# Kernel optimization log

Hardware: AMD Instinct MI355X
Metric: run time of the kernel (lower is better)

Reference implementation:

```python
import jax, jax.numpy as jnp
import numpy as np
import math

B, S, D, H = 2, 1024, 1024, 16
DH = D // H
BUCKETS, MAXPOS = 256, 512
SPAN = BUCKETS  # pos_ebd_size (att_span)


def make_log_bucket_position(rel, bucket_size, max_position):
    sign = jnp.sign(rel).astype(jnp.float32)
    mid = bucket_size // 2
    abs_pos = jnp.where((rel < mid) & (rel > -mid), mid - 1, jnp.abs(rel)).astype(jnp.float32)
    log_pos = jnp.ceil(jnp.log(abs_pos / mid) / np.log((max_position - 1) / mid) * (mid - 1)) + mid
    return jnp.where(abs_pos <= mid, rel.astype(jnp.float32), log_pos * sign).astype(jnp.int32)


def build_relative_position(q_size, k_size):
    rel = jnp.arange(q_size, dtype=jnp.int32)[:, None] - jnp.arange(k_size, dtype=jnp.int32)[None, :]
    return make_log_bucket_position(rel, BUCKETS, MAXPOS)


def setup_inputs() -> dict:
    key = jax.random.key(0)
    ks = jax.random.split(key, 8)
    w = lambda k: jax.random.normal(k, (D, D), dtype=jnp.float32) * 0.02
    return {
        "hidden_states": jax.random.normal(ks[0], (B, S, D), dtype=jnp.float32),
        "attention_mask": jnp.ones((B, 1, S, S), dtype=jnp.int32),
        "rel_embeddings": jax.random.normal(ks[1], (2 * SPAN, D), dtype=jnp.float32),
        "Wq": w(ks[2]), "bq": jnp.zeros((D,), jnp.float32),
        "Wk": w(ks[3]), "bk": jnp.zeros((D,), jnp.float32),
        "Wv": w(ks[4]), "bv": jnp.zeros((D,), jnp.float32),
    }


def reference(hidden_states, attention_mask, rel_embeddings, Wq, bq, Wk, bk, Wv, bv):
    split = lambda x: x.reshape(B, -1, H, DH).transpose(0, 2, 1, 3)  # [B,H,S,dh]
    q = split(hidden_states @ Wq + bq)
    k = split(hidden_states @ Wk + bk)
    v = split(hidden_states @ Wv + bv)

    SCALE_FACTOR = 3  # 1 + c2p + p2c
    scale = math.sqrt(DH * SCALE_FACTOR)
    scores = jnp.einsum('bhqd,bhkd->bhqk', q, k) / scale

    # disentangled relative-position bias (share_att_key=True -> reuse q/k proj)
    re = rel_embeddings[: 2 * SPAN]  # [2*SPAN, D]
    pos_q = (re @ Wq + bq).reshape(2 * SPAN, H, DH).transpose(1, 0, 2)  # [H,P,dh]
    pos_k = (re @ Wk + bk).reshape(2 * SPAN, H, DH).transpose(1, 0, 2)

    rel_pos = build_relative_position(S, S)  # [S,S] bucketized

    # c2p: gather along the position axis per (q,k) pair
    c2p_pos = jnp.clip(rel_pos + SPAN, 0, 2 * SPAN - 1)
    c2p_att = jnp.einsum('bhqd,hpd->bhqp', q, pos_k)  # [B,H,S,2*SPAN]
    c2p = jnp.take_along_axis(c2p_att, c2p_pos[None, None], axis=-1)  # [B,H,S,S]

    # p2c: gather for key positions, then transpose back to [q,k]
    p2c_pos = jnp.clip(-rel_pos + SPAN, 0, 2 * SPAN - 1)
    p2c_att = jnp.einsum('bhkd,hpd->bhkp', k, pos_q)
    p2c = jnp.swapaxes(jnp.take_along_axis(p2c_att, p2c_pos[None, None], axis=-1), -1, -2)

    scores = scores + (c2p + p2c) / scale

    # XSoftmax: masked fill -> softmax -> zero masked
    valid = attention_mask.astype(bool)
    scores = jnp.where(valid, scores, jnp.finfo(scores.dtype).min)
    probs = jax.nn.softmax(scores, axis=-1)
    probs = jnp.where(valid, probs, 0.0)

    ctx = jnp.einsum('bhqk,bhkd->bhqd', probs, v)
    return ctx.transpose(0, 2, 1, 3).reshape(B, S, D)
```

## Files before the change

### kernel.cpp

```cpp
#include <hip/hip_runtime.h>
#include <hip/hip_bf16.h>
#include <math.h>

#define B_   2
#define S_   1024
#define D_   1024
#define H_   16
#define DH_  64
#define P_   512

#define SCALE2 (0.07216878364870323f * 1.4426950408889634f)

typedef __bf16 bf16;
typedef __bf16 bf16x8 __attribute__((ext_vector_type(8)));
typedef __bf16 bf16x4 __attribute__((ext_vector_type(4)));
typedef float  f32x4  __attribute__((ext_vector_type(4)));

__device__ __forceinline__ f32x4 mfma16(bf16x8 a, bf16x8 b, f32x4 c) {
  return __builtin_amdgcn_mfma_f32_16x16x32_bf16(a, b, c, 0, 0, 0);
}

__device__ __forceinline__ bf16x8 ld8(const bf16* p) {
  return *reinterpret_cast<const bf16x8*>(p);
}

__device__ __forceinline__ void gl_lds16(const void* g, void* l) {
  __builtin_amdgcn_global_load_lds(
      (const __attribute__((address_space(1))) void*)g,
      (__attribute__((address_space(3))) void*)l, 16, 0, 0);
}

__device__ __forceinline__ bf16x8 ld8f(const float* p) {
  const f32x4* pv = reinterpret_cast<const f32x4*>(p);
  f32x4 lo = pv[0], hi = pv[1];
  bf16x8 r;
#pragma unroll
  for (int j = 0; j < 4; j++) { r[j] = (bf16)lo[j]; r[4 + j] = (bf16)hi[j]; }
  return r;
}

__global__ __launch_bounds__(256)
void k_prep(const float* __restrict__ hidden, const float* __restrict__ re,
            const float* __restrict__ Wq, const float* __restrict__ Wk,
            const float* __restrict__ Wv,
            bf16* __restrict__ Xc, int* __restrict__ ci, bf16* __restrict__ Wt) {
  __shared__ bf16 tile[64][72];
  const int bx = blockIdx.x;
  const int t = threadIdx.x;
  if (bx < 1280) {
    int gt = bx * 256 + t;
    if (gt < 2047) {
      int rel = gt - 1023;
      int sgn = (rel > 0) - (rel < 0);
      float abs_pos = (rel < 128 && rel > -128) ? 127.0f : fabsf((float)rel);
      int bucket;
      if (abs_pos <= 128.0f) {
        bucket = rel;
      } else {
        const float logden = 1.3843393302355437f;
        float t1 = logf(abs_pos * (1.0f / 128.0f));
        float lp = ceilf(t1 / logden * 127.0f) + 128.0f;
        bucket = (int)lp * sgn;
      }
      ci[gt] = min(max(bucket + 256, 0), 511);
    }
    size_t i8 = (size_t)gt * 8;
    const size_t HN = (size_t)2048 * 1024;
    const float* src = (i8 < HN) ? (hidden + i8) : (re + (i8 - HN));
    *reinterpret_cast<bf16x8*>(&Xc[i8]) = ld8f(src);
    return;
  }
  const int bid2 = bx - 1280;
  const int w = bid2 >> 8;
  const int rem = bid2 & 255;
  const int n0 = (rem & 15) * 64;
  const int k0 = (rem >> 4) * 64;
  const float* W = (w == 0) ? Wq : (w == 1) ? Wk : Wv;
  bf16* Out = Wt + (size_t)w * D_ * D_;
  {
    const int row = t >> 2, c0 = (t & 3) * 16;
    bf16x8 v0 = ld8f(W + (size_t)(k0 + row) * D_ + n0 + c0);
    bf16x8 v1 = ld8f(W + (size_t)(k0 + row) * D_ + n0 + c0 + 8);
    *reinterpret_cast<bf16x8*>(&tile[row][c0]) = v0;
    *reinterpret_cast<bf16x8*>(&tile[row][c0 + 8]) = v1;
  }
  __syncthreads();
  {
    const int nr = t >> 2, kc0 = (t & 3) * 16;
    bf16x8 o0, o1;
#pragma unroll
    for (int j = 0; j < 8; j++) o0[j] = tile[kc0 + j][nr];
#pragma unroll
    for (int j = 0; j < 8; j++) o1[j] = tile[kc0 + 8 + j][nr];
    *reinterpret_cast<bf16x8*>(&Out[(size_t)(n0 + nr) * D_ + k0 + kc0]) = o0;
    *reinterpret_cast<bf16x8*>(&Out[(size_t)(n0 + nr) * D_ + k0 + kc0 + 8]) = o1;
  }
}

__global__ __launch_bounds__(512)
void k_proj(const bf16* __restrict__ Xc, const bf16* __restrict__ Wt,
            const float* __restrict__ bq, const float* __restrict__ bk,
            const float* __restrict__ bv,
            bf16* __restrict__ qb, bf16* __restrict__ kb, bf16* __restrict__ vbT,
            bf16* __restrict__ posq, bf16* __restrict__ posk) {
  __shared__ __align__(16) char smem[65536];
  bf16* As = reinterpret_cast<bf16*>(smem);
  bf16* Bs = reinterpret_cast<bf16*>(smem + 32768);
  const int t = threadIdx.x;
  const int w = t >> 6, lane = t & 63, quad = lane >> 4, lc = lane & 15;
  const int wm = w >> 2, wn = w & 3;
  const int m0 = blockIdx.y * 128;
  const int wsel = blockIdx.x >> 3;
  const int n0 = (blockIdx.x & 7) * 128;
  if (wsel == 2 && m0 >= 2048) return;
  const bf16* WtW = Wt + (size_t)wsel * D_ * D_;
  const float* bias = (wsel == 0) ? bq : (wsel == 1) ? bk : bv;
  const bf16* Agl = Xc + (size_t)m0 * D_;
  const bf16* Bgl = WtW + (size_t)n0 * D_;

  int rS[4], cS[4];
#pragma unroll
  for (int i = 0; i < 4; i++) {
    int g = i * 512 + t;
    rS[i] = g >> 4;
    cS[i] = (g & 15) ^ (rS[i] & 15);
  }

  f32x4 zv = {0.f, 0.f, 0.f, 0.f};
  f32x4 acc[4][2];
#pragma unroll
  for (int i = 0; i < 4; i++)
#pragma unroll
    for (int j = 0; j < 2; j++) acc[i][j] = zv;

  for (int k0 = 0; k0 < D_; k0 += 128) {
#pragma unroll
    for (int i = 0; i < 4; i++)
      gl_lds16(Agl + (size_t)rS[i] * D_ + k0 + cS[i] * 8,
               &As[(i * 512 + w * 64) * 8]);
#pragma unroll
    for (int i = 0; i < 4; i++)
      gl_lds16(Bgl + (size_t)rS[i] * D_ + k0 + cS[i] * 8,
               &Bs[(i * 512 + w * 64) * 8]);
    __syncthreads();

#pragma unroll
    for (int h = 0; h < 4; h++) {
      bf16x8 af[4], bfr[2];
#pragma unroll
      for (int mt = 0; mt < 4; mt++) {
        int row = wm * 64 + mt * 16 + lc;
        int ch = (h * 4 + quad) ^ (row & 15);
        af[mt] = ld8(&As[row * 128 + ch * 8]);
      }
#pragma unroll
      for (int nt = 0; nt < 2; nt++) {
        int row = wn * 32 + nt * 16 + lc;
        int ch = (h * 4 + quad) ^ (row & 15);
        bfr[nt] = ld8(&Bs[row * 128 + ch * 8]);
      }
#pragma unroll
      for (int mt = 0; mt < 4; mt++)
#pragma unroll
        for (int nt = 0; nt < 2; nt++)
          acc[mt][nt] = mfma16(af[mt], bfr[nt], acc[mt][nt]);
    }
    __syncthreads();
  }

  if (wsel == 2) {
#pragma unroll
    for (int nt = 0; nt < 2; nt++) {
      int nl = n0 + wn * 32 + nt * 16 + lc;
      float bsv = bias[nl];
      int h = nl >> 6, d = nl & 63;
#pragma unroll
      for (int mt = 0; mt < 4; mt++) {
        int i0 = m0 + wm * 64 + mt * 16 + quad * 4;
        int b = i0 >> 10, s0 = i0 & 1023;
        int spos = (s0 & ~63) | (quad * 16 + mt * 4);
        bf16x4 ov;
#pragma unroll
        for (int r = 0; r < 4; r++) ov[r] = (bf16)(acc[mt][nt][r] + bsv);
        *reinterpret_cast<bf16x4*>(
            &vbT[(((size_t)(b * H_ + h)) * DH_ + d) * S_ + spos]) = ov;
      }
    }
  } else {
    bf16* Cl = reinterpret_cast<bf16*>(smem);
#pragma unroll
    for (int nt = 0; nt < 2; nt++) {
      int nl = n0 + wn * 32 + nt * 16 + lc;
      float bsv = bias[nl];
      int jl = wn * 32 + nt * 16 + lc;
#pragma unroll
      for (int mt = 0; mt < 4; mt++) {
#pragma unroll
        for (int r = 0; r < 4; r++) {
          int il = wm * 64 + mt * 16 + quad * 4 + r;
          Cl[il * 136 + jl] = (bf16)(acc[mt][nt][r] + bsv);
        }
      }
    }
    __syncthreads();
    const int hg = t >> 8;
    const int tl = t & 255;
    const int hglob = (n0 >> 6) + hg;
    bf16* dst;
    if (m0 < 2048) {
      int b = m0 >> 10, s0 = m0 & 1023;
      bf16* qk = (wsel == 0) ? qb : kb;
      dst = qk + (((size_t)(b * H_ + hglob)) * S_ + s0) * DH_;
    } else {
      int p0 = m0 - 2048;
      bf16* pm = (wsel == 0) ? posq : posk;
      dst = pm + ((size_t)hglob * P_ + p0) * DH_;
    }
#pragma unroll
    for (int rep = 0; rep < 4; rep++) {
      int u = rep * 256 + tl;
      int sl = u >> 3, dc = u & 7;
      bf16x8 v = *reinterpret_cast<const bf16x8*>(
          &Cl[sl * 136 + hg * 64 + dc * 8]);
      *reinterpret_cast<bf16x8*>(&dst[(size_t)u * 8]) = v;
    }
  }
}

__global__ __launch_bounds__(256)
void k_rel(const bf16* __restrict__ qb, const bf16* __restrict__ kb,
           const bf16* __restrict__ posq, const bf16* __restrict__ posk,
           bf16* __restrict__ c2p, bf16* __restrict__ p2c,
           const int* __restrict__ ci) {
  const int t = threadIdx.x;
  const int w = t >> 6, lane = t & 63, quad = lane >> 4, lc = lane & 15;
  const int which = blockIdx.z & 1;
  const int bh = blockIdx.z >> 1;
  const int h = bh & (H_ - 1);
  const int q0 = blockIdx.x * 64;
  const bf16* QK = (which ? kb : qb) + (size_t)bh * S_ * DH_;
  const bf16* PM = (which ? posq : posk) + (size_t)h * P_ * DH_;
  bf16* Out = (which ? p2c : c2p) + (size_t)bh * S_ * P_;

  int lo8, hi8;
  if (which == 0) { lo8 = ci[q0] & ~7;        hi8 = (ci[q0 + 960] & ~7) + 135; }
  else            { lo8 = ci[960 - q0] & ~7;  hi8 = (ci[1920 - q0] & ~7) + 135; }

  f32x4 zv = {0.f, 0.f, 0.f, 0.f};
  bf16x8 bq[4][2];
#pragma unroll
  for (int qi = 0; qi < 4; qi++) {
    const bf16* qp = QK + (size_t)(q0 + qi * 16 + lc) * DH_ + quad * 8;
    bq[qi][0] = ld8(qp);
    bq[qi][1] = ld8(qp + 32);
  }
  const int p0 = w * 128;
#pragma unroll 2
  for (int pt = 0; pt < 8; pt++) {
    const int pb = p0 + pt * 16;
    if (pb + 15 < lo8 || pb > hi8) continue;
    const bf16* pp = PM + (size_t)(pb + lc) * DH_ + quad * 8;
    bf16x8 pa0 = ld8(pp), pa1 = ld8(pp + 32);
#pragma unroll
    for (int qi = 0; qi < 4; qi++) {
      f32x4 acc = mfma16(pa1, bq[qi][1], mfma16(pa0, bq[qi][0], zv));
      int q = q0 + qi * 16 + lc;
      int pbase = pb + quad * 4;
      bf16x4 ov;
#pragma unroll
      for (int r = 0; r < 4; r++) ov[r] = (bf16)acc[r];
      *reinterpret_cast<bf16x4*>(&Out[(size_t)q * P_ + pbase]) = ov;
    }
  }
}

__global__ __launch_bounds__(256, 2)
void k_attn(const bf16* __restrict__ qb, const bf16* __restrict__ kb,
            const bf16* __restrict__ vbT, const bf16* __restrict__ c2p,
            const bf16* __restrict__ p2c, const int* __restrict__ citab,
            float* __restrict__ out) {
  __shared__ bf16 c2pS[64 * 136];
  __shared__ bf16 p2cS[64 * 136];
  __shared__ bf16 vT0[64 * 64];
  __shared__ bf16 vT1[64 * 64];
  __shared__ int  ciT[2048];

  const int t = threadIdx.x;
  const int w = t >> 6, lane = t & 63, quad = lane >> 4, lc = lane & 15;
  const int bh = blockIdx.x;
  const int q0 = blockIdx.y * 64;

  const bf16* qp = qb + ((size_t)bh * S_ + q0 + w * 16 + lc) * DH_ + quad * 8;
  bf16x8 aq0 = ld8(qp), aq1 = ld8(qp + 32);

  const bf16* kbB = kb + (size_t)bh * S_ * DH_;
  const bf16* vbB = vbT + (size_t)bh * DH_ * S_;
  const bf16* c2pB = c2p + (size_t)bh * S_ * P_;
  const bf16* p2cB = p2c + (size_t)bh * S_ * P_;

#pragma unroll
  for (int i = 0; i < 2; i++)
    gl_lds16((const char*)citab + (size_t)(i * 256 + t) * 16,
             (char*)ciT + (i * 256 + w * 64) * 16);

  int wrow[5], wch[5];
#pragma unroll
  for (int i = 0; i < 5; i++) {
    int slot = i * 256 + ((i == 4) ? (t & 63) : t);
    wrow[i] = slot / 17;
    wch[i] = slot - wrow[i] * 17;
  }
  int vrow[2], vch[2];
#pragma unroll
  for (int i = 0; i < 2; i++) {
    int slot = i * 256 + t;
    vrow[i] = slot >> 3;
    vch[i] = (slot & 7) ^ (vrow[i] & 7);
  }

  f32x4 zv = {0.f, 0.f, 0.f, 0.f};
  float m_r = -INFINITY, l_r = 0.f;
  f32x4 oacc[4];
#pragma unroll
  for (int dg = 0; dg < 4; dg++) oacc[dg] = zv;

  const int jbase2 = w * 16 + lc + 63 - quad * 4;
  const int qoff = (w * 16 + lc) * 136;
  int poff[4];
#pragma unroll
  for (int g = 0; g < 4; g++) poff[g] = (g * 16 + quad * 4) * 136;

  __syncthreads();

  int clo8_cur = ciT[q0 + 960] & ~7;
#pragma unroll
  for (int i = 0; i < 4; i++) {
    gl_lds16(c2pB + (size_t)(q0 + wrow[i]) * P_ + clo8_cur + wch[i] * 8,
             &c2pS[(i * 256 + w * 64) * 8]);
    gl_lds16(p2cB + (size_t)(0 + wrow[i]) * P_ + clo8_cur + wch[i] * 8,
             &p2cS[(i * 256 + w * 64) * 8]);
  }
  if (w == 0) {
    gl_lds16(c2pB + (size_t)(q0 + wrow[4]) * P_ + clo8_cur + wch[4] * 8,
             &c2pS[1024 * 8]);
    gl_lds16(p2cB + (size_t)(0 + wrow[4]) * P_ + clo8_cur + wch[4] * 8,
             &p2cS[1024 * 8]);
  }
#pragma unroll
  for (int i = 0; i < 2; i++)
    gl_lds16(vbB + (size_t)vrow[i] * S_ + 0 + vch[i] * 8,
             &vT0[(i * 256 + w * 64) * 8]);

  f32x4 rc[5], rp[5], rv[2];
  {
    const int clo81 = ciT[q0 + 896] & ~7;
#pragma unroll
    for (int i = 0; i < 4; i++) {
      rc[i] = *reinterpret_cast<const f32x4*>(
          c2pB + (size_t)(q0 + wrow[i]) * P_ + clo81 + wch[i] * 8);
      rp[i] = *reinterpret_cast<const f32x4*>(
          p2cB + (size_t)(64 + wrow[i]) * P_ + clo81 + wch[i] * 8);
    }
    if (w == 0) {
      rc[4] = *reinterpret_cast<const f32x4*>(
          c2pB + (size_t)(q0 + wrow[4]) * P_ + clo81 + wch[4] * 8);
      rp[4] = *reinterpret_cast<const f32x4*>(
          p2cB + (size_t)(64 + wrow[4]) * P_ + clo81 + wch[4] * 8);
    }
#pragma unroll
    for (int i = 0; i < 2; i++)
      rv[i] = *reinterpret_cast<const f32x4*>(
          vbB + (size_t)vrow[i] * S_ + 64 + vch[i] * 8);
  }

  bf16x8 kf[4][2];
#pragma unroll
  for (int g = 0; g < 4; g++) {
    const bf16* kp = kbB + (size_t)(g * 16 + lc) * DH_ + quad * 8;
    kf[g][0] = ld8(kp);
    kf[g][1] = ld8(kp + 32);
  }

  int buf = 0;
  for (int kt = 0; kt < S_; kt += 64) {
    __syncthreads();

    int idxn = q0 - kt + 896;
    const int clo8n = ciT[idxn < 0 ? 0 : idxn] & ~7;

    const int ktn = (kt + 64 < S_) ? kt + 64 : 0;
    bf16x8 kfn[4][2];
#pragma unroll
    for (int g = 0; g < 4; g++) {
      const bf16* kp = kbB + (size_t)(ktn + g * 16 + lc) * DH_ + quad * 8;
      kfn[g][0] = ld8(kp);
      kfn[g][1] = ld8(kp + 32);
    }

    f32x4 s[4];
#pragma unroll
    for (int g = 0; g < 4; g++)
      s[g] = mfma16(kf[g][1], aq1, mfma16(kf[g][0], aq0, zv));

    const int jb = q0 - kt + 960 + jbase2;
    int jj[4][4];
#pragma unroll
    for (int g = 0; g < 4; g++)
#pragma unroll
      for (int r = 0; r < 4; r++)
        jj[g][r] = ciT[jb - 16 * g - r] - clo8_cur;
    float cvv[4][4], pvv[4][4];
#pragma unroll
    for (int g = 0; g < 4; g++)
#pragma unroll
      for (int r = 0; r < 4; r++) {
        cvv[g][r] = (float)c2pS[qoff + jj[g][r]];
        pvv[g][r] = (float)p2cS[poff[g] + r * 136 + jj[g][r]];
      }
#pragma unroll
    for (int g = 0; g < 4; g++)
#pragma unroll
      for (int r = 0; r < 4; r++)
        s[g][r] = (s[g][r] + cvv[g][r] + pvv[g][r]) * SCALE2;

    __syncthreads();

    if (kt + 64 < S_) {
      bf16* vnext = buf ? vT0 : vT1;
#pragma unroll
      for (int i = 0; i < 4; i++) {
        *reinterpret_cast<f32x4*>(&c2pS[(i * 256 + t) * 8]) = rc[i];
        *reinterpret_cast<f32x4*>(&p2cS[(i * 256 + t) * 8]) = rp[i];
      }
      if (w == 0) {
        *reinterpret_cast<f32x4*>(&c2pS[(1024 + (t & 63)) * 8]) = rc[4];
        *reinterpret_cast<f32x4*>(&p2cS[(1024 + (t & 63)) * 8]) = rp[4];
      }
#pragma unroll
      for (int i = 0; i < 2; i++)
        *reinterpret_cast<f32x4*>(&vnext[(i * 256 + t) * 8]) = rv[i];
    }

    const bf16* vcur = buf ? vT1 : vT0;
    bf16x8 va0a[4], va1a[4];
#pragma unroll
    for (int dg = 0; dg < 4; dg++) {
      int row = dg * 16 + lc;
      va0a[dg] = ld8(&vcur[row * 64 + ((2 * quad) ^ (row & 7)) * 8]);
      va1a[dg] = ld8(&vcur[row * 64 + ((2 * quad + 1) ^ (row & 7)) * 8]);
    }

    if (kt + 128 < S_) {
      const int kv2 = kt + 128;
      const int clo82 = ciT[q0 - kt + 832] & ~7;
#pragma unroll
      for (int i = 0; i < 4; i++) {
        rc[i] = *reinterpret_cast<const f32x4*>(
            c2pB + (size_t)(q0 + wrow[i]) * P_ + clo82 + wch[i] * 8);
        rp[i] = *reinterpret_cast<const f32x4*>(
            p2cB + (size_t)(kv2 + wrow[i]) * P_ + clo82 + wch[i] * 8);
      }
      if (w == 0) {
        rc[4] = *reinterpret_cast<const f32x4*>(
            c2pB + (size_t)(q0 + wrow[4]) * P_ + clo82 + wch[4] * 8);
        rp[4] = *reinterpret_cast<const f32x4*>(
            p2cB + (size_t)(kv2 + wrow[4]) * P_ + clo82 + wch[4] * 8);
      }
#pragma unroll
      for (int i = 0; i < 2; i++)
        rv[i] = *reinterpret_cast<const f32x4*>(
            vbB + (size_t)vrow[i] * S_ + kv2 + vch[i] * 8);
    }

    float mx;
    {
      float m0 = fmaxf(fmaxf(s[0][0], s[0][1]), fmaxf(s[0][2], s[0][3]));
      float m1 = fmaxf(fmaxf(s[1][0], s[1][1]), fmaxf(s[1][2], s[1][3]));
      float m2 = fmaxf(fmaxf(s[2][0], s[2][1]), fmaxf(s[2][2], s[2][3]));
      float m3 = fmaxf(fmaxf(s[3][0], s[3][1]), fmaxf(s[3][2], s[3][3]));
      mx = fmaxf(fmaxf(m0, m1), fmaxf(m2, m3));
    }
    mx = fmaxf(mx, __shfl_xor(mx, 16));
    mx = fmaxf(mx, __shfl_xor(mx, 32));
    float mnew = fmaxf(m_r, mx);
    float alpha = exp2f(m_r - mnew);
    m_r = mnew;
    float ps = 0.f;
#pragma unroll
    for (int g = 0; g < 4; g++)
#pragma unroll
      for (int r = 0; r < 4; r++) {
        float pe = exp2f(s[g][r] - mnew);
        s[g][r] = pe;
        ps += pe;
      }
    ps += __shfl_xor(ps, 16);
    ps += __shfl_xor(ps, 32);
    l_r = l_r * alpha + ps;
#pragma unroll
    for (int dg = 0; dg < 4; dg++)
#pragma unroll
      for (int r = 0; r < 4; r++) oacc[dg][r] *= alpha;

    bf16x8 pb0, pb1;
#pragma unroll
    for (int e = 0; e < 8; e++) {
      pb0[e] = (bf16)s[e >> 2][e & 3];
      pb1[e] = (bf16)s[2 + (e >> 2)][e & 3];
    }

#pragma unroll
    for (int dg = 0; dg < 4; dg++)
      oacc[dg] = mfma16(va1a[dg], pb1, mfma16(va0a[dg], pb0, oacc[dg]));

    clo8_cur = clo8n;
#pragma unroll
    for (int g = 0; g < 4; g++) { kf[g][0] = kfn[g][0]; kf[g][1] = kfn[g][1]; }
    buf ^= 1;
  }

  const int b = bh >> 4, h = bh & 15;
  const float inv = 1.0f / l_r;
  const int qa = q0 + w * 16 + lc;
#pragma unroll
  for (int dg = 0; dg < 4; dg++) {
    f32x4 ov;
#pragma unroll
    for (int r = 0; r < 4; r++) ov[r] = oacc[dg][r] * inv;
    *reinterpret_cast<f32x4*>(
        &out[((size_t)(b * S_) + qa) * D_ + h * DH_ + dg * 16 + quad * 4]) = ov;
  }
}

extern "C" void kernel_launch(void* const* d_in, const int* in_sizes, int n_in,
                              void* d_out, int out_size, void* d_ws,
                              size_t ws_size, hipStream_t stream) {
  const float* hidden = (const float*)d_in[0];
  const float* re = (const float*)d_in[2];
  const float* Wq = (const float*)d_in[3];
  const float* bq = (const float*)d_in[4];
  const float* Wk = (const float*)d_in[5];
  const float* bk = (const float*)d_in[6];
  const float* Wv = (const float*)d_in[7];
  const float* bv = (const float*)d_in[8];

  char* ws = (char*)d_ws;
  const size_t MB = 1024 * 1024;
  bf16* qb   = (bf16*)(ws + 0 * MB);
  bf16* kb   = (bf16*)(ws + 4 * MB);
  bf16* vbT  = (bf16*)(ws + 8 * MB);
  bf16* posq = (bf16*)(ws + 12 * MB);
  bf16* posk = (bf16*)(ws + 13 * MB);
  int*  ci   = (int*) (ws + 14 * MB);
  bf16* Wt   = (bf16*)(ws + 15 * MB);
  bf16* c2p  = (bf16*)(ws + 26 * MB);
  bf16* p2c  = (bf16*)(ws + 58 * MB);
  bf16* Xc   = (bf16*)(ws + 26 * MB);
  if (ws_size < 92 * MB) return;

  k_prep<<<dim3(2048), dim3(256), 0, stream>>>(hidden, re, Wq, Wk, Wv,
                                               Xc, ci, Wt);
  k_proj<<<dim3(24, 20), dim3(512), 0, stream>>>(Xc, Wt, bq, bk, bv,
                                                 qb, kb, vbT, posq, posk);
  k_rel<<<dim3(16, 1, 64), dim3(256), 0, stream>>>(qb, kb, posq, posk,
                                                   c2p, p2c, ci);
  k_attn<<<dim3(32, 16), dim3(256), 0, stream>>>(qb, kb, vbT, c2p, p2c, ci,
                                                 (float*)d_out);
}
```

Before: 190.6 us.

## Process two query tiles per attention block sharing p2c and V tiles

The attention kernel now runs 512 threads per block covering 128 queries as two 64-query tiles, so the p2c window and the V tile for each key block are loaded once and shared by both. The p2c LDS window is widened to 200 columns to span both tiles' offset ranges. The register-staged double-buffered prefetch of c2p/p2c/V is replaced by direct global-to-LDS async loads issued one iteration ahead, and the bucket index table is stored as 16-bit to shrink its LDS footprint. The intent is to cut redundant global traffic and register pressure, at the cost of roughly 80KB of dynamic LDS per block, lower block-level occupancy, and less latency hiding from the shorter prefetch distance.

```diff
diff --git a/kernel.cpp b/kernel.cpp
--- a/kernel.cpp
+++ b/kernel.cpp
@@ -43,7 +43,8 @@
 void k_prep(const float* __restrict__ hidden, const float* __restrict__ re,
             const float* __restrict__ Wq, const float* __restrict__ Wk,
             const float* __restrict__ Wv,
-            bf16* __restrict__ Xc, int* __restrict__ ci, bf16* __restrict__ Wt) {
+            bf16* __restrict__ Xc, int* __restrict__ ci,
+            unsigned short* __restrict__ ci16, bf16* __restrict__ Wt) {
   __shared__ bf16 tile[64][72];
   const int bx = blockIdx.x;
   const int t = threadIdx.x;
@@ -62,7 +63,9 @@
         float lp = ceilf(t1 / logden * 127.0f) + 128.0f;
         bucket = (int)lp * sgn;
       }
-      ci[gt] = min(max(bucket + 256, 0), 511);
+      int v = min(max(bucket + 256, 0), 511);
+      ci[gt] = v;
+      ci16[gt] = (unsigned short)v;
     }
     size_t i8 = (size_t)gt * 8;
     const size_t HN = (size_t)2048 * 1024;
@@ -274,23 +277,27 @@
   }
 }
 
-__global__ __launch_bounds__(256, 2)
+__global__ __launch_bounds__(512)
 void k_attn(const bf16* __restrict__ qb, const bf16* __restrict__ kb,
             const bf16* __restrict__ vbT, const bf16* __restrict__ c2p,
-            const bf16* __restrict__ p2c, const int* __restrict__ citab,
+            const bf16* __restrict__ p2c,
+            const unsigned short* __restrict__ ci16,
             float* __restrict__ out) {
-  __shared__ bf16 c2pS[64 * 136];
-  __shared__ bf16 p2cS[64 * 136];
-  __shared__ bf16 vT0[64 * 64];
-  __shared__ bf16 vT1[64 * 64];
-  __shared__ int  ciT[2048];
+  extern __shared__ char smem[];
+  bf16* c2pS = reinterpret_cast<bf16*>(smem);
+  bf16* p2cS = reinterpret_cast<bf16*>(smem + 34816);
+  bf16* vT0  = reinterpret_cast<bf16*>(smem + 60416);
+  bf16* vT1  = reinterpret_cast<bf16*>(smem + 68608);
+  unsigned short* ciT = reinterpret_cast<unsigned short*>(smem + 76800);
 
   const int t = threadIdx.x;
   const int w = t >> 6, lane = t & 63, quad = lane >> 4, lc = lane & 15;
+  const int qt = w >> 2, sub = w & 3;
   const int bh = blockIdx.x;
-  const int q0 = blockIdx.y * 64;
-
-  const bf16* qp = qb + ((size_t)bh * S_ + q0 + w * 16 + lc) * DH_ + quad * 8;
+  const int q0p = blockIdx.y * 128;
+  const int q0 = q0p + qt * 64;
+
+  const bf16* qp = qb + ((size_t)bh * S_ + q0 + sub * 16 + lc) * DH_ + quad * 8;
   bf16x8 aq0 = ld8(qp), aq1 = ld8(qp + 32);
 
   const bf16* kbB = kb + (size_t)bh * S_ * DH_;
@@ -298,25 +305,40 @@
   const bf16* c2pB = c2p + (size_t)bh * S_ * P_;
   const bf16* p2cB = p2c + (size_t)bh * S_ * P_;
 
-#pragma unroll
-  for (int i = 0; i < 2; i++)
-    gl_lds16((const char*)citab + (size_t)(i * 256 + t) * 16,
-             (char*)ciT + (i * 256 + w * 64) * 16);
-
-  int wrow[5], wch[5];
-#pragma unroll
-  for (int i = 0; i < 5; i++) {
-    int slot = i * 256 + ((i == 4) ? (t & 63) : t);
-    wrow[i] = slot / 17;
-    wch[i] = slot - wrow[i] * 17;
-  }
-  int vrow[2], vch[2];
-#pragma unroll
-  for (int i = 0; i < 2; i++) {
-    int slot = i * 256 + t;
-    vrow[i] = slot >> 3;
-    vch[i] = (slot & 7) ^ (vrow[i] & 7);
-  }
+  if (t < 256)
+    gl_lds16((const char*)ci16 + (size_t)t * 16, (char*)ciT + (t >> 6) * 1024);
+
+  int crow[4], cch[4], ctsel[4], cslb[4];
+#pragma unroll
+  for (int i = 0; i < 4; i++) {
+    int s = i * 512 + t;
+    ctsel[i] = (s >= 1088);
+    int sl = s - (ctsel[i] ? 1088 : 0);
+    crow[i] = sl / 17;
+    cch[i] = sl - crow[i] * 17;
+    cslb[i] = (i * 512 + (t & ~63)) - (ctsel[i] ? 1088 : 0);
+  }
+  int c4row = 0, c4ch = 0, c4slb = 0;
+  if (t < 128) {
+    int sl = 960 + t;
+    c4row = sl / 17;
+    c4ch = sl - c4row * 17;
+    c4slb = 960 + (t & 64);
+  }
+  int prow[3], pch[3];
+#pragma unroll
+  for (int i = 0; i < 3; i++) {
+    int s = i * 512 + t;
+    prow[i] = s / 25;
+    pch[i] = s - prow[i] * 25;
+  }
+  int p3row = 0, p3ch = 0;
+  if (t < 64) {
+    int s = 1536 + t;
+    p3row = s / 25;
+    p3ch = s - p3row * 25;
+  }
+  const int vrow = t >> 3, vch = (t & 7) ^ (vrow & 7);
 
   f32x4 zv = {0.f, 0.f, 0.f, 0.f};
   float m_r = -INFINITY, l_r = 0.f;
@@ -324,54 +346,34 @@
 #pragma unroll
   for (int dg = 0; dg < 4; dg++) oacc[dg] = zv;
 
-  const int jbase2 = w * 16 + lc + 63 - quad * 4;
-  const int qoff = (w * 16 + lc) * 136;
+  const int jbase2 = sub * 16 + lc + 63 - quad * 4;
+  const int qbase = qt * 8704 + (sub * 16 + lc) * 136;
   int poff[4];
 #pragma unroll
-  for (int g = 0; g < 4; g++) poff[g] = (g * 16 + quad * 4) * 136;
+  for (int g = 0; g < 4; g++) poff[g] = (g * 16 + quad * 4) * 200;
 
   __syncthreads();
 
-  int clo8_cur = ciT[q0 + 960] & ~7;
-#pragma unroll
-  for (int i = 0; i < 4; i++) {
-    gl_lds16(c2pB + (size_t)(q0 + wrow[i]) * P_ + clo8_cur + wch[i] * 8,
-             &c2pS[(i * 256 + w * 64) * 8]);
-    gl_lds16(p2cB + (size_t)(0 + wrow[i]) * P_ + clo8_cur + wch[i] * 8,
-             &p2cS[(i * 256 + w * 64) * 8]);
-  }
-  if (w == 0) {
-    gl_lds16(c2pB + (size_t)(q0 + wrow[4]) * P_ + clo8_cur + wch[4] * 8,
-             &c2pS[1024 * 8]);
-    gl_lds16(p2cB + (size_t)(0 + wrow[4]) * P_ + clo8_cur + wch[4] * 8,
-             &p2cS[1024 * 8]);
-  }
-#pragma unroll
-  for (int i = 0; i < 2; i++)
-    gl_lds16(vbB + (size_t)vrow[i] * S_ + 0 + vch[i] * 8,
-             &vT0[(i * 256 + w * 64) * 8]);
-
-  f32x4 rc[5], rp[5], rv[2];
-  {
-    const int clo81 = ciT[q0 + 896] & ~7;
-#pragma unroll
-    for (int i = 0; i < 4; i++) {
-      rc[i] = *reinterpret_cast<const f32x4*>(
-          c2pB + (size_t)(q0 + wrow[i]) * P_ + clo81 + wch[i] * 8);
-      rp[i] = *reinterpret_cast<const f32x4*>(
-          p2cB + (size_t)(64 + wrow[i]) * P_ + clo81 + wch[i] * 8);
-    }
-    if (w == 0) {
-      rc[4] = *reinterpret_cast<const f32x4*>(
-          c2pB + (size_t)(q0 + wrow[4]) * P_ + clo81 + wch[4] * 8);
-      rp[4] = *reinterpret_cast<const f32x4*>(
-          p2cB + (size_t)(64 + wrow[4]) * P_ + clo81 + wch[4] * 8);
-    }
-#pragma unroll
-    for (int i = 0; i < 2; i++)
-      rv[i] = *reinterpret_cast<const f32x4*>(
-          vbB + (size_t)vrow[i] * S_ + 64 + vch[i] * 8);
-  }
+  int cloA[2];
+  cloA[0] = ((int)ciT[q0p + 960]) & ~7;
+  cloA[1] = ((int)ciT[q0p + 64 + 960]) & ~7;
+
+#pragma unroll
+  for (int i = 0; i < 4; i++)
+    gl_lds16(c2pB + (size_t)(q0p + ctsel[i] * 64 + crow[i]) * P_ +
+                 cloA[ctsel[i]] + cch[i] * 8,
+             (char*)c2pS + ctsel[i] * 17408 + cslb[i] * 16);
+  if (t < 128)
+    gl_lds16(c2pB + (size_t)(q0p + 64 + c4row) * P_ + cloA[1] + c4ch * 8,
+             (char*)c2pS + 17408 + c4slb * 16);
+#pragma unroll
+  for (int i = 0; i < 3; i++)
+    gl_lds16(p2cB + (size_t)(0 + prow[i]) * P_ + cloA[0] + pch[i] * 8,
+             (char*)p2cS + (i * 512 + (t & ~63)) * 16);
+  if (t < 64)
+    gl_lds16(p2cB + (size_t)(0 + p3row) * P_ + cloA[0] + p3ch * 8,
+             (char*)p2cS + 1536 * 16);
+  gl_lds16(vbB + (size_t)vrow * S_ + 0 + vch * 8, (char*)vT0 + (t & ~63) * 16);
 
   bf16x8 kf[4][2];
 #pragma unroll
@@ -385,8 +387,13 @@
   for (int kt = 0; kt < S_; kt += 64) {
     __syncthreads();
 
-    int idxn = q0 - kt + 896;
-    const int clo8n = ciT[idxn < 0 ? 0 : idxn] & ~7;
+    int cloN[2];
+    {
+      int i0 = q0p - kt + 896;
+      int i1 = q0p + 64 - kt + 896;
+      cloN[0] = ((int)ciT[i0 < 0 ? 0 : i0]) & ~7;
+      cloN[1] = ((int)ciT[i1 < 0 ? 0 : i1]) & ~7;
+    }
 
     const int ktn = (kt + 64 < S_) ? kt + 64 : 0;
     bf16x8 kfn[4][2];
@@ -403,19 +410,19 @@
       s[g] = mfma16(kf[g][1], aq1, mfma16(kf[g][0], aq0, zv));
 
     const int jb = q0 - kt + 960 + jbase2;
-    int jj[4][4];
+    int cvt[4][4];
 #pragma unroll
     for (int g = 0; g < 4; g++)
 #pragma unroll
       for (int r = 0; r < 4; r++)
-        jj[g][r] = ciT[jb - 16 * g - r] - clo8_cur;
+        cvt[g][r] = (int)ciT[jb - 16 * g - r];
     float cvv[4][4], pvv[4][4];
 #pragma unroll
     for (int g = 0; g < 4; g++)
 #pragma unroll
       for (int r = 0; r < 4; r++) {
-        cvv[g][r] = (float)c2pS[qoff + jj[g][r]];
-        pvv[g][r] = (float)p2cS[poff[g] + r * 136 + jj[g][r]];
+        cvv[g][r] = (float)c2pS[qbase + (cvt[g][r] - cloA[qt])];
+        pvv[g][r] = (float)p2cS[poff[g] + r * 200 + (cvt[g][r] - cloA[0])];
       }
 #pragma unroll
     for (int g = 0; g < 4; g++)
@@ -427,18 +434,24 @@
 
     if (kt + 64 < S_) {
       bf16* vnext = buf ? vT0 : vT1;
-#pragma unroll
-      for (int i = 0; i < 4; i++) {
-        *reinterpret_cast<f32x4*>(&c2pS[(i * 256 + t) * 8]) = rc[i];
-        *reinterpret_cast<f32x4*>(&p2cS[(i * 256 + t) * 8]) = rp[i];
-      }
-      if (w == 0) {
-        *reinterpret_cast<f32x4*>(&c2pS[(1024 + (t & 63)) * 8]) = rc[4];
-        *reinterpret_cast<f32x4*>(&p2cS[(1024 + (t & 63)) * 8]) = rp[4];
-      }
-#pragma unroll
-      for (int i = 0; i < 2; i++)
-        *reinterpret_cast<f32x4*>(&vnext[(i * 256 + t) * 8]) = rv[i];
+      const int kn = kt + 64;
+#pragma unroll
+      for (int i = 0; i < 4; i++)
+        gl_lds16(c2pB + (size_t)(q0p + ctsel[i] * 64 + crow[i]) * P_ +
+                     cloN[ctsel[i]] + cch[i] * 8,
+                 (char*)c2pS + ctsel[i] * 17408 + cslb[i] * 16);
+      if (t < 128)
+        gl_lds16(c2pB + (size_t)(q0p + 64 + c4row) * P_ + cloN[1] + c4ch * 8,
+                 (char*)c2pS + 17408 + c4slb * 16);
+#pragma unroll
+      for (int i = 0; i < 3; i++)
+        gl_lds16(p2cB + (size_t)(kn + prow[i]) * P_ + cloN[0] + pch[i] * 8,
+                 (char*)p2cS + (i * 512 + (t & ~63)) * 16);
+      if (t < 64)
+        gl_lds16(p2cB + (size_t)(kn + p3row) * P_ + cloN[0] + p3ch * 8,
+                 (char*)p2cS + 1536 * 16);
+      gl_lds16(vbB + (size_t)vrow * S_ + kn + vch * 8,
+               (char*)vnext + (t & ~63) * 16);
     }
 
     const bf16* vcur = buf ? vT1 : vT0;
@@ -448,28 +461,6 @@
       int row = dg * 16 + lc;
       va0a[dg] = ld8(&vcur[row * 64 + ((2 * quad) ^ (row & 7)) * 8]);
       va1a[dg] = ld8(&vcur[row * 64 + ((2 * quad + 1) ^ (row & 7)) * 8]);
-    }
-
-    if (kt + 128 < S_) {
-      const int kv2 = kt + 128;
-      const int clo82 = ciT[q0 - kt + 832] & ~7;
-#pragma unroll
-      for (int i = 0; i < 4; i++) {
-        rc[i] = *reinterpret_cast<const f32x4*>(
-            c2pB + (size_t)(q0 + wrow[i]) * P_ + clo82 + wch[i] * 8);
-        rp[i] = *reinterpret_cast<const f32x4*>(
-            p2cB + (size_t)(kv2 + wrow[i]) * P_ + clo82 + wch[i] * 8);
-      }
-      if (w == 0) {
-        rc[4] = *reinterpret_cast<const f32x4*>(
-            c2pB + (size_t)(q0 + wrow[4]) * P_ + clo82 + wch[4] * 8);
-        rp[4] = *reinterpret_cast<const f32x4*>(
-            p2cB + (size_t)(kv2 + wrow[4]) * P_ + clo82 + wch[4] * 8);
-      }
-#pragma unroll
-      for (int i = 0; i < 2; i++)
-        rv[i] = *reinterpret_cast<const f32x4*>(
-            vbB + (size_t)vrow[i] * S_ + kv2 + vch[i] * 8);
     }
 
     float mx;
@@ -513,7 +504,8 @@
     for (int dg = 0; dg < 4; dg++)
       oacc[dg] = mfma16(va1a[dg], pb1, mfma16(va0a[dg], pb0, oacc[dg]));
 
-    clo8_cur = clo8n;
+    cloA[0] = cloN[0];
+    cloA[1] = cloN[1];
 #pragma unroll
     for (int g = 0; g < 4; g++) { kf[g][0] = kfn[g][0]; kf[g][1] = kfn[g][1]; }
     buf ^= 1;
@@ -521,7 +513,7 @@
 
   const int b = bh >> 4, h = bh & 15;
   const float inv = 1.0f / l_r;
-  const int qa = q0 + w * 16 + lc;
+  const int qa = q0 + sub * 16 + lc;
 #pragma unroll
   for (int dg = 0; dg < 4; dg++) {
     f32x4 ov;
@@ -552,18 +544,26 @@
   bf16* posq = (bf16*)(ws + 12 * MB);
   bf16* posk = (bf16*)(ws + 13 * MB);
   int*  ci   = (int*) (ws + 14 * MB);
+  unsigned short* ci16 = (unsigned short*)(ws + 14 * MB + 32768);
   bf16* Wt   = (bf16*)(ws + 15 * MB);
   bf16* c2p  = (bf16*)(ws + 26 * MB);
   bf16* p2c  = (bf16*)(ws + 58 * MB);
   bf16* Xc   = (bf16*)(ws + 26 * MB);
   if (ws_size < 92 * MB) return;
 
+  static bool attr_done = false;
+  if (!attr_done) {
+    hipFuncSetAttribute((const void*)k_attn,
+                        hipFuncAttributeMaxDynamicSharedMemorySize, 81920);
+    attr_done = true;
+  }
+
   k_prep<<<dim3(2048), dim3(256), 0, stream>>>(hidden, re, Wq, Wk, Wv,
-                                               Xc, ci, Wt);
+                                               Xc, ci, ci16, Wt);
   k_proj<<<dim3(24, 20), dim3(512), 0, stream>>>(Xc, Wt, bq, bk, bv,
                                                  qb, kb, vbT, posq, posk);
   k_rel<<<dim3(16, 1, 64), dim3(256), 0, stream>>>(qb, kb, posq, posk,
                                                    c2p, p2c, ci);
-  k_attn<<<dim3(32, 16), dim3(256), 0, stream>>>(qb, kb, vbT, c2p, p2c, ci,
-                                                 (float*)d_out);
-}
+  k_attn<<<dim3(32, 8), dim3(512), 80896, stream>>>(qb, kb, vbT, c2p, p2c,
+                                                    ci16, (float*)d_out);
+}
```

Result: slower. 195.5 us (+2.6%).
